# Kernel optimization log

Hardware: AMD Instinct MI355X
Metric: run time of the kernel (lower is better)

Reference implementation:

```python
import jax, jax.numpy as jnp
import numpy as np

D_MODEL = 4096
D_BASE = 8192
K_SUB = 1024
N_TOK = 8192


def setup_inputs() -> dict:
    key = jax.random.key(0)
    k1, k2, k3, k4 = jax.random.split(key, 4)
    x = jax.random.normal(k1, (N_TOK, D_MODEL), dtype=jnp.float32)
    subspace_indices = jax.random.randint(k2, (K_SUB,), 0, D_BASE)
    # learned shared basis (orthogonal init approximated by scaled gaussian)
    U_base = jax.random.normal(k3, (D_MODEL, D_BASE), dtype=jnp.float32) / np.sqrt(D_MODEL)
    V_base = jax.random.normal(k4, (D_BASE, D_MODEL), dtype=jnp.float32) / np.sqrt(D_BASE)
    return {"x": x, "subspace_indices": subspace_indices, "U_base": U_base, "V_base": V_base}


def reference(x, subspace_indices, U_base, V_base):
    # gather active subspace columns/rows of the shared basis
    u_subset = U_base[:, subspace_indices]          # [d_model, k]
    v_subset = V_base[subspace_indices, :]          # [k, d_model]
    projected = jax.nn.silu(x @ u_subset)           # [n_tok, k]
    return projected @ v_subset                     # [n_tok, d_model]
```

## Files before the change

### kernel.cpp

```cpp
#include <hip/hip_runtime.h>
#include <hip/hip_bf16.h>
#include <stdint.h>

#define D_MODEL 4096
#define D_BASE  8192
#define K_SUB   1024
#define N_TOK   8192

typedef __attribute__((ext_vector_type(8))) short bf16x8;
typedef __attribute__((ext_vector_type(4))) float f32x4;

__device__ __forceinline__ unsigned short f2bf(float f) {
    union { float f; uint32_t u; } c; c.f = f;
    uint32_t u = c.u;
    uint32_t r = u + 0x7FFFu + ((u >> 16) & 1u);
    return (unsigned short)(r >> 16);
}

__device__ __forceinline__ void gload_lds16(const void* g, void* l) {
    __builtin_amdgcn_global_load_lds(
        (__attribute__((address_space(1))) void*)g,
        (__attribute__((address_space(3))) void*)l, 16, 0, 0);
}

#define VMCNT(N) do { __builtin_amdgcn_sched_barrier(0); \
    asm volatile("s_waitcnt vmcnt(" #N ")" ::: "memory"); } while (0)
#define PHASE_MID() do { __builtin_amdgcn_sched_barrier(0); __builtin_amdgcn_s_barrier(); \
    asm volatile("s_waitcnt lgkmcnt(0)" ::: "memory"); __builtin_amdgcn_sched_barrier(0); } while (0)
#define PHASE_END() do { __builtin_amdgcn_sched_barrier(0); __builtin_amdgcn_s_barrier(); } while (0)

__global__ void convert_x_kernel(const float* __restrict__ x, unsigned short* __restrict__ xb) {
    int t = blockIdx.x * 256 + threadIdx.x;
    const float4* p = (const float4*)x + (size_t)t * 2;
    float4 a = p[0], b = p[1];
    ushort4 lo, hi;
    lo.x = f2bf(a.x); lo.y = f2bf(a.y); lo.z = f2bf(a.z); lo.w = f2bf(a.w);
    hi.x = f2bf(b.x); hi.y = f2bf(b.y); hi.z = f2bf(b.z); hi.w = f2bf(b.w);
    *(ushort4*)(xb + (size_t)t * 8) = lo;
    *(ushort4*)(xb + (size_t)t * 8 + 4) = hi;
}

__global__ __launch_bounds__(256) void gather_u_s(const float* __restrict__ U,
                                                  const int* __restrict__ idx,
                                                  unsigned short* __restrict__ Ut) {
    __shared__ unsigned short tile[1024 * 36];
    __shared__ int lidx[1024];
    const int t = threadIdx.x;
    const int k0 = blockIdx.x * 32;
    #pragma unroll
    for (int i = 0; i < 4; ++i) lidx[i * 256 + t] = idx[i * 256 + t];
    __syncthreads();
    for (int kr = 0; kr < 32; ++kr) {
        const float* Urow = U + (size_t)(k0 + kr) * D_BASE;
        #pragma unroll
        for (int it = 0; it < 4; ++it) {
            int n = it * 256 + t;
            tile[n * 36 + kr] = f2bf(Urow[lidx[n]]);
        }
    }
    __syncthreads();
    #pragma unroll
    for (int r = 0; r < 4; ++r) {
        int n = r * 256 + t;
        unsigned short* drow = Ut + (size_t)n * D_MODEL + k0;
        #pragma unroll
        for (int j = 0; j < 8; ++j) {
            ushort4 v = *(const ushort4*)&tile[n * 36 + j * 4];
            *(ushort4*)(drow + j * 4) = v;
        }
    }
}

__global__ __launch_bounds__(256) void gather_v_t(const float* __restrict__ V,
                                                  const int* __restrict__ idx,
                                                  unsigned short* __restrict__ Vt) {
    __shared__ unsigned short tile[64][66];
    __shared__ int lidx[64];
    const int t = threadIdx.x;
    const int n0 = (blockIdx.x & 15) * 64;
    const int d0 = (blockIdx.x >> 4) * 64;
    if (t < 64) lidx[t] = idx[n0 + t];
    __syncthreads();
    const int c = t & 63, r4 = t >> 6;
    #pragma unroll
    for (int p = 0; p < 16; ++p) {
        int nr = p * 4 + r4;
        tile[nr][c] = f2bf(V[(size_t)lidx[nr] * D_MODEL + d0 + c]);
    }
    __syncthreads();
    #pragma unroll
    for (int p = 0; p < 16; ++p) {
        int dr = p * 4 + r4;
        Vt[(size_t)(d0 + dr) * K_SUB + n0 + c] = tile[c][dr];
    }
}

__global__ __launch_bounds__(512, 2)
void gemm1_8p(const unsigned short* __restrict__ A, const unsigned short* __restrict__ Bt,
              unsigned short* __restrict__ C) {
    constexpr int K = D_MODEL, N = K_SUB, NT = K / 64;
    __shared__ __align__(16) unsigned short lds[49152];

    const int t = threadIdx.x, lane = t & 63, w = t >> 6;
    const int wm = w >> 1, wn = w & 1;
    const int lr = lane & 15, lk = lane >> 4;

    const int f = blockIdx.x;
    const int g = (f & 7) * 32 + (f >> 3);
    const int m0 = (g >> 3) * 256, n0 = (g & 7) * 128;

    const int cswz0 = ((lk ^ (lr & 7)) * 8);
    const int cswz1 = (((4 + lk) ^ (lr & 7)) * 8);
    const int srow = lane >> 3;
    const int scol = ((lane & 7) ^ srow) * 8;

    auto stage_A = [&](int kt, int half) {
        const unsigned short* src = A + (size_t)(m0 + half * 128) * K + kt * 64;
        unsigned short* dst = &lds[(kt & 1) * 24576 + half * 8192];
        #pragma unroll
        for (int i = 0; i < 2; ++i) {
            int c2 = i * 8 + w;
            gload_lds16(src + (size_t)(c2 * 8 + srow) * K + scol, dst + c2 * 512);
        }
    };
    auto stage_B = [&](int kt) {
        const unsigned short* src = Bt + (size_t)n0 * K + kt * 64;
        unsigned short* dst = &lds[(kt & 1) * 24576 + 16384];
        #pragma unroll
        for (int i = 0; i < 2; ++i) {
            int c2 = i * 8 + w;
            gload_lds16(src + (size_t)(c2 * 8 + srow) * K + scol, dst + c2 * 512);
        }
    };
    auto read_A = [&](int kt, bf16x8 (&af)[4][2]) {
        const unsigned short* base = &lds[(kt & 1) * 24576 + (wm >> 1) * 8192];
        #pragma unroll
        for (int m = 0; m < 4; ++m) {
            int rw = (wm & 1) * 64 + m * 16 + lr;
            af[m][0] = *(const bf16x8*)(base + rw * 64 + cswz0);
            af[m][1] = *(const bf16x8*)(base + rw * 64 + cswz1);
        }
    };
    auto read_B2 = [&](int kt, int nh, bf16x8 (&bfr)[2][2]) {
        const unsigned short* base = &lds[(kt & 1) * 24576 + 16384];
        #pragma unroll
        for (int n = 0; n < 2; ++n) {
            int rw = wn * 64 + (nh * 2 + n) * 16 + lr;
            bfr[n][0] = *(const bf16x8*)(base + rw * 64 + cswz0);
            bfr[n][1] = *(const bf16x8*)(base + rw * 64 + cswz1);
        }
    };

    f32x4 acc[4][4] = {};

    stage_A(0, 0); stage_A(0, 1); stage_B(0); stage_A(1, 0);
    VMCNT(2);
    __builtin_amdgcn_s_barrier();
    __builtin_amdgcn_sched_barrier(0);

    for (int kt = 0; kt < NT; kt += 2) {
        const bool more = (kt + 2 < NT);
        {
            bf16x8 af[4][2], bfr[2][2];
            read_A(kt, af); read_B2(kt, 0, bfr);
            stage_A(kt + 1, 1); stage_B(kt + 1);
            PHASE_MID();
            __builtin_amdgcn_s_setprio(1);
            #pragma unroll
            for (int m = 0; m < 4; ++m)
                #pragma unroll
                for (int n = 0; n < 2; ++n)
                    #pragma unroll
                    for (int ks = 0; ks < 2; ++ks)
                        acc[m][n] = __builtin_amdgcn_mfma_f32_16x16x32_bf16(
                            af[m][ks], bfr[n][ks], acc[m][n], 0, 0, 0);
            __builtin_amdgcn_s_setprio(0);
            PHASE_END();
            bf16x8 bfr2[2][2];
            read_B2(kt, 1, bfr2);
            if (more) stage_A(kt + 2, 0);
            PHASE_MID();
            __builtin_amdgcn_s_setprio(1);
            #pragma unroll
            for (int m = 0; m < 4; ++m)
                #pragma unroll
                for (int n = 0; n < 2; ++n)
                    #pragma unroll
                    for (int ks = 0; ks < 2; ++ks)
                        acc[m][2 + n] = __builtin_amdgcn_mfma_f32_16x16x32_bf16(
                            af[m][ks], bfr2[n][ks], acc[m][2 + n], 0, 0, 0);
            __builtin_amdgcn_s_setprio(0);
            if (more) { VMCNT(2); } else { VMCNT(0); }
            PHASE_END();
        }
        {
            bf16x8 af[4][2], bfr[2][2];
            read_A(kt + 1, af); read_B2(kt + 1, 0, bfr);
            if (more) { stage_A(kt + 2, 1); stage_B(kt + 2); }
            PHASE_MID();
            __builtin_amdgcn_s_setprio(1);
            #pragma unroll
            for (int m = 0; m < 4; ++m)
                #pragma unroll
                for (int n = 0; n < 2; ++n)
                    #pragma unroll
                    for (int ks = 0; ks < 2; ++ks)
                        acc[m][n] = __builtin_amdgcn_mfma_f32_16x16x32_bf16(
                            af[m][ks], bfr[n][ks], acc[m][n], 0, 0, 0);
            __builtin_amdgcn_s_setprio(0);
            PHASE_END();
            bf16x8 bfr2[2][2];
            read_B2(kt + 1, 1, bfr2);
            if (more) stage_A(kt + 3, 0);
            PHASE_MID();
            __builtin_amdgcn_s_setprio(1);
            #pragma unroll
            for (int m = 0; m < 4; ++m)
                #pragma unroll
                for (int n = 0; n < 2; ++n)
                    #pragma unroll
                    for (int ks = 0; ks < 2; ++ks)
                        acc[m][2 + n] = __builtin_amdgcn_mfma_f32_16x16x32_bf16(
                            af[m][ks], bfr2[n][ks], acc[m][2 + n], 0, 0, 0);
            __builtin_amdgcn_s_setprio(0);
            if (more) VMCNT(2);
            PHASE_END();
        }
    }

    #pragma unroll
    for (int m = 0; m < 4; ++m)
        #pragma unroll
        for (int n = 0; n < 4; ++n)
            #pragma unroll
            for (int r = 0; r < 4; ++r) {
                int row = m0 + wm * 64 + m * 16 + lk * 4 + r;
                int col = n0 + wn * 64 + n * 16 + lr;
                float v = acc[m][n][r];
                v = v / (1.0f + __expf(-v));
                C[(size_t)row * N + col] = f2bf(v);
            }
}

__global__ __launch_bounds__(512, 2)
void gemm2_8p(const unsigned short* __restrict__ A, const unsigned short* __restrict__ Bt,
              float* __restrict__ C) {
    constexpr int K = K_SUB, N = D_MODEL, NT = K / 64;
    constexpr int BUFSZ = 32768;
    __shared__ __align__(16) unsigned short lds[2 * BUFSZ];

    const int t = threadIdx.x, lane = t & 63, w = t >> 6;
    const int wr = w >> 2, wc = w & 3;
    const int lr = lane & 15, lk = lane >> 4;

    const int f = blockIdx.x;
    const int g = (f & 7) * 64 + (f >> 3);
    const int m0 = (g >> 4) * 256, n0 = (g & 15) * 256;

    const int cswz0 = ((lk ^ (lr & 7)) * 8);
    const int cswz1 = (((4 + lk) ^ (lr & 7)) * 8);
    const int srow = lane >> 3;
    const int scol = ((lane & 7) ^ srow) * 8;

    auto stage_A = [&](int kt, int mh) {
        const unsigned short* src = A + (size_t)(m0 + mh * 128) * K + kt * 64;
        unsigned short* dst = &lds[(kt & 1) * BUFSZ + mh * 8192];
        #pragma unroll
        for (int i = 0; i < 2; ++i) {
            int c2 = i * 8 + w;
            gload_lds16(src + (size_t)(c2 * 8 + srow) * K + scol, dst + c2 * 512);
        }
    };
    auto stage_B = [&](int kt, int nh) {
        const unsigned short* src = Bt + (size_t)(n0 + nh * 128) * K + kt * 64;
        unsigned short* dst = &lds[(kt & 1) * BUFSZ + 16384 + nh * 8192];
        #pragma unroll
        for (int i = 0; i < 2; ++i) {
            int c2 = i * 8 + w;
            gload_lds16(src + (size_t)(c2 * 8 + srow) * K + scol, dst + c2 * 512);
        }
    };
    auto read_A = [&](int kt, int mh, bf16x8 (&af)[4][2]) {
        const unsigned short* base = &lds[(kt & 1) * BUFSZ + mh * 8192];
        #pragma unroll
        for (int m = 0; m < 4; ++m) {
            int rw = wr * 64 + m * 16 + lr;
            af[m][0] = *(const bf16x8*)(base + rw * 64 + cswz0);
            af[m][1] = *(const bf16x8*)(base + rw * 64 + cswz1);
        }
    };
    auto read_B = [&](int kt, int nh, bf16x8 (&bfr)[2][2]) {
        const unsigned short* base = &lds[(kt & 1) * BUFSZ + 16384 + nh * 8192];
        #pragma unroll
        for (int n = 0; n < 2; ++n) {
            int rw = wc * 32 + n * 16 + lr;
            bfr[n][0] = *(const bf16x8*)(base + rw * 64 + cswz0);
            bfr[n][1] = *(const bf16x8*)(base + rw * 64 + cswz1);
        }
    };

    f32x4 acc[8][4] = {};

    stage_A(0, 0); stage_B(0, 0); stage_B(0, 1); stage_A(0, 1);
    stage_A(1, 0); stage_B(1, 1); stage_A(1, 1);
    VMCNT(6);
    __builtin_amdgcn_s_barrier();
    __builtin_amdgcn_sched_barrier(0);

    for (int kt = 0; kt < NT; ++kt) {
        bf16x8 af[4][2], bf0[2][2], bf1[2][2];
        {
            read_A(kt, 0, af); read_B(kt, 0, bf0);
            if (kt + 1 < NT) stage_B(kt + 1, 0);
            PHASE_MID();
            __builtin_amdgcn_s_setprio(1);
            #pragma unroll
            for (int m = 0; m < 4; ++m)
                #pragma unroll
                for (int n = 0; n < 2; ++n)
                    #pragma unroll
                    for (int ks = 0; ks < 2; ++ks)
                        acc[m][n] = __builtin_amdgcn_mfma_f32_16x16x32_bf16(
                            af[m][ks], bf0[n][ks], acc[m][n], 0, 0, 0);
            __builtin_amdgcn_s_setprio(0);
            PHASE_END();
        }
        {
            read_B(kt, 1, bf1);
            if (kt + 2 < NT) stage_A(kt + 2, 0);
            PHASE_MID();
            __builtin_amdgcn_s_setprio(1);
            #pragma unroll
            for (int m = 0; m < 4; ++m)
                #pragma unroll
                for (int n = 0; n < 2; ++n)
                    #pragma unroll
                    for (int ks = 0; ks < 2; ++ks)
                        acc[m][2 + n] = __builtin_amdgcn_mfma_f32_16x16x32_bf16(
                            af[m][ks], bf1[n][ks], acc[m][2 + n], 0, 0, 0);
            __builtin_amdgcn_s_setprio(0);
            PHASE_END();
        }
        {
            read_A(kt, 1, af);
            if (kt + 2 < NT) stage_B(kt + 2, 1);
            PHASE_MID();
            __builtin_amdgcn_s_setprio(1);
            #pragma unroll
            for (int m = 0; m < 4; ++m)
                #pragma unroll
                for (int n = 0; n < 2; ++n)
                    #pragma unroll
                    for (int ks = 0; ks < 2; ++ks)
                        acc[4 + m][n] = __builtin_amdgcn_mfma_f32_16x16x32_bf16(
                            af[m][ks], bf0[n][ks], acc[4 + m][n], 0, 0, 0);
            __builtin_amdgcn_s_setprio(0);
            PHASE_END();
        }
        {
            if (kt + 2 < NT) stage_A(kt + 2, 1);
            PHASE_MID();
            __builtin_amdgcn_s_setprio(1);
            #pragma unroll
            for (int m = 0; m < 4; ++m)
                #pragma unroll
                for (int n = 0; n < 2; ++n)
                    #pragma unroll
                    for (int ks = 0; ks < 2; ++ks)
                        acc[4 + m][2 + n] = __builtin_amdgcn_mfma_f32_16x16x32_bf16(
                            af[m][ks], bf1[n][ks], acc[4 + m][2 + n], 0, 0, 0);
            __builtin_amdgcn_s_setprio(0);
            __builtin_amdgcn_sched_barrier(0);
            if (kt < NT - 2) { VMCNT(6); }
            else if (kt == NT - 2) { VMCNT(0); }
            PHASE_END();
        }
    }

    #pragma unroll
    for (int mh = 0; mh < 2; ++mh)
        #pragma unroll
        for (int nh = 0; nh < 2; ++nh)
            #pragma unroll
            for (int m = 0; m < 4; ++m)
                #pragma unroll
                for (int n = 0; n < 2; ++n)
                    #pragma unroll
                    for (int r = 0; r < 4; ++r) {
                        int row = m0 + mh * 128 + wr * 64 + m * 16 + lk * 4 + r;
                        int col = n0 + nh * 128 + wc * 32 + n * 16 + lr;
                        C[(size_t)row * N + col] = acc[mh * 4 + m][nh * 2 + n][r];
                    }
}

extern "C" void kernel_launch(void* const* d_in, const int* in_sizes, int n_in,
                              void* d_out, int out_size, void* d_ws, size_t ws_size,
                              hipStream_t stream) {
    const float* x   = (const float*)d_in[0];
    const int*   idx = (const int*)d_in[1];
    const float* U   = (const float*)d_in[2];
    const float* V   = (const float*)d_in[3];
    float* out = (float*)d_out;

    unsigned short* Ut = (unsigned short*)d_ws;
    unsigned short* Vt = Ut + (size_t)K_SUB * D_MODEL;
    unsigned short* P  = Vt + (size_t)K_SUB * D_MODEL;
    unsigned short* xb = (unsigned short*)d_out;

    convert_x_kernel<<<(N_TOK * D_MODEL) / (256 * 8), 256, 0, stream>>>(x, xb);
    gather_u_s<<<D_MODEL / 32, 256, 0, stream>>>(U, idx, Ut);
    gather_v_t<<<(K_SUB / 64) * (D_MODEL / 64), 256, 0, stream>>>(V, idx, Vt);

    gemm1_8p<<<256, 512, 0, stream>>>(xb, Ut, P);
    gemm2_8p<<<512, 512, 0, stream>>>(P, Vt, out);
}
```

Baseline: 241.8 us.

## Switch GEMMs to 32x32x16 MFMA and fuse prep kernels into one launch

Both GEMM kernels replace the 16x16x32 bf16 MFMA tiles with 32x32x16 tiles, changing the LDS fragment reads, accumulator layout and epilogue indexing to match. The three preprocessing kernels (x conversion, U gather, V gather-transpose) are merged into a single launch dispatched by block index. The U gather is also rewritten to drop its LDS staging and write 4-element vectors directly. The aim is fewer MFMA issues and operand reads per FLOP and less launch overhead. In exchange, the U gather now does strided uncoalesced reads, and the larger accumulators raise register pressure.

```diff
diff --git a/kernel.cpp b/kernel.cpp
--- a/kernel.cpp
+++ b/kernel.cpp
@@ -8,7 +8,7 @@
 #define N_TOK   8192
 
 typedef __attribute__((ext_vector_type(8))) short bf16x8;
-typedef __attribute__((ext_vector_type(4))) float f32x4;
+typedef __attribute__((ext_vector_type(16))) float f32x16;
 
 __device__ __forceinline__ unsigned short f2bf(float f) {
     union { float f; uint32_t u; } c; c.f = f;
@@ -29,69 +29,60 @@
     asm volatile("s_waitcnt lgkmcnt(0)" ::: "memory"); __builtin_amdgcn_sched_barrier(0); } while (0)
 #define PHASE_END() do { __builtin_amdgcn_sched_barrier(0); __builtin_amdgcn_s_barrier(); } while (0)
 
-__global__ void convert_x_kernel(const float* __restrict__ x, unsigned short* __restrict__ xb) {
-    int t = blockIdx.x * 256 + threadIdx.x;
-    const float4* p = (const float4*)x + (size_t)t * 2;
-    float4 a = p[0], b = p[1];
-    ushort4 lo, hi;
-    lo.x = f2bf(a.x); lo.y = f2bf(a.y); lo.z = f2bf(a.z); lo.w = f2bf(a.w);
-    hi.x = f2bf(b.x); hi.y = f2bf(b.y); hi.z = f2bf(b.z); hi.w = f2bf(b.w);
-    *(ushort4*)(xb + (size_t)t * 8) = lo;
-    *(ushort4*)(xb + (size_t)t * 8 + 4) = hi;
-}
-
-__global__ __launch_bounds__(256) void gather_u_s(const float* __restrict__ U,
+__global__ __launch_bounds__(256) void prep_fused(const float* __restrict__ x,
                                                   const int* __restrict__ idx,
-                                                  unsigned short* __restrict__ Ut) {
-    __shared__ unsigned short tile[1024 * 36];
-    __shared__ int lidx[1024];
-    const int t = threadIdx.x;
-    const int k0 = blockIdx.x * 32;
-    #pragma unroll
-    for (int i = 0; i < 4; ++i) lidx[i * 256 + t] = idx[i * 256 + t];
-    __syncthreads();
-    for (int kr = 0; kr < 32; ++kr) {
-        const float* Urow = U + (size_t)(k0 + kr) * D_BASE;
-        #pragma unroll
-        for (int it = 0; it < 4; ++it) {
-            int n = it * 256 + t;
-            tile[n * 36 + kr] = f2bf(Urow[lidx[n]]);
-        }
-    }
-    __syncthreads();
-    #pragma unroll
-    for (int r = 0; r < 4; ++r) {
-        int n = r * 256 + t;
-        unsigned short* drow = Ut + (size_t)n * D_MODEL + k0;
-        #pragma unroll
-        for (int j = 0; j < 8; ++j) {
-            ushort4 v = *(const ushort4*)&tile[n * 36 + j * 4];
-            *(ushort4*)(drow + j * 4) = v;
-        }
-    }
-}
-
-__global__ __launch_bounds__(256) void gather_v_t(const float* __restrict__ V,
-                                                  const int* __restrict__ idx,
+                                                  const float* __restrict__ U,
+                                                  const float* __restrict__ V,
+                                                  unsigned short* __restrict__ xb,
+                                                  unsigned short* __restrict__ Ut,
                                                   unsigned short* __restrict__ Vt) {
     __shared__ unsigned short tile[64][66];
     __shared__ int lidx[64];
+    const int b = blockIdx.x;
     const int t = threadIdx.x;
-    const int n0 = (blockIdx.x & 15) * 64;
-    const int d0 = (blockIdx.x >> 4) * 64;
-    if (t < 64) lidx[t] = idx[n0 + t];
-    __syncthreads();
-    const int c = t & 63, r4 = t >> 6;
-    #pragma unroll
-    for (int p = 0; p < 16; ++p) {
-        int nr = p * 4 + r4;
-        tile[nr][c] = f2bf(V[(size_t)lidx[nr] * D_MODEL + d0 + c]);
-    }
-    __syncthreads();
-    #pragma unroll
-    for (int p = 0; p < 16; ++p) {
-        int dr = p * 4 + r4;
-        Vt[(size_t)(d0 + dr) * K_SUB + n0 + c] = tile[c][dr];
+    if (b < 256) {
+        const int nq = t >> 2, kq = t & 3;
+        const int k0 = b * 16 + kq * 4;
+        #pragma unroll
+        for (int c = 0; c < 16; ++c) {
+            int n = nq + 64 * c;
+            int col = idx[n];
+            const float* Ucol = U + (size_t)k0 * D_BASE + col;
+            ushort4 o;
+            o.x = f2bf(Ucol[0]);
+            o.y = f2bf(Ucol[(size_t)D_BASE]);
+            o.z = f2bf(Ucol[(size_t)2 * D_BASE]);
+            o.w = f2bf(Ucol[(size_t)3 * D_BASE]);
+            *(ushort4*)(Ut + (size_t)n * D_MODEL + k0) = o;
+        }
+    } else if (b < 256 + 1024) {
+        const int bx = b - 256;
+        const int n0 = (bx & 15) * 64;
+        const int d0 = (bx >> 4) * 64;
+        if (t < 64) lidx[t] = idx[n0 + t];
+        __syncthreads();
+        const int c = t & 63, r4 = t >> 6;
+        #pragma unroll
+        for (int p = 0; p < 16; ++p) {
+            int nr = p * 4 + r4;
+            tile[nr][c] = f2bf(V[(size_t)lidx[nr] * D_MODEL + d0 + c]);
+        }
+        __syncthreads();
+        #pragma unroll
+        for (int p = 0; p < 16; ++p) {
+            int dr = p * 4 + r4;
+            Vt[(size_t)(d0 + dr) * K_SUB + n0 + c] = tile[c][dr];
+        }
+    } else {
+        const int cb = b - 1280;
+        int e = cb * 256 + t;
+        const float4* p = (const float4*)x + (size_t)e * 2;
+        float4 a = p[0], q = p[1];
+        ushort4 lo, hi;
+        lo.x = f2bf(a.x); lo.y = f2bf(a.y); lo.z = f2bf(a.z); lo.w = f2bf(a.w);
+        hi.x = f2bf(q.x); hi.y = f2bf(q.y); hi.z = f2bf(q.z); hi.w = f2bf(q.w);
+        *(ushort4*)(xb + (size_t)e * 8) = lo;
+        *(ushort4*)(xb + (size_t)e * 8 + 4) = hi;
     }
 }
 
@@ -103,14 +94,12 @@
 
     const int t = threadIdx.x, lane = t & 63, w = t >> 6;
     const int wm = w >> 1, wn = w & 1;
-    const int lr = lane & 15, lk = lane >> 4;
+    const int l31 = lane & 31, lh = lane >> 5;
 
     const int f = blockIdx.x;
     const int g = (f & 7) * 32 + (f >> 3);
     const int m0 = (g >> 3) * 256, n0 = (g & 7) * 128;
 
-    const int cswz0 = ((lk ^ (lr & 7)) * 8);
-    const int cswz1 = (((4 + lk) ^ (lr & 7)) * 8);
     const int srow = lane >> 3;
     const int scol = ((lane & 7) ^ srow) * 8;
 
@@ -132,26 +121,29 @@
             gload_lds16(src + (size_t)(c2 * 8 + srow) * K + scol, dst + c2 * 512);
         }
     };
-    auto read_A = [&](int kt, bf16x8 (&af)[4][2]) {
+    auto read_A = [&](int kt, bf16x8 (&af)[2][4]) {
         const unsigned short* base = &lds[(kt & 1) * 24576 + (wm >> 1) * 8192];
         #pragma unroll
-        for (int m = 0; m < 4; ++m) {
-            int rw = (wm & 1) * 64 + m * 16 + lr;
-            af[m][0] = *(const bf16x8*)(base + rw * 64 + cswz0);
-            af[m][1] = *(const bf16x8*)(base + rw * 64 + cswz1);
-        }
-    };
-    auto read_B2 = [&](int kt, int nh, bf16x8 (&bfr)[2][2]) {
+        for (int mf = 0; mf < 2; ++mf) {
+            int rw = (wm & 1) * 64 + mf * 32 + l31;
+            #pragma unroll
+            for (int ks = 0; ks < 4; ++ks) {
+                int gg = ks * 2 + lh;
+                af[mf][ks] = *(const bf16x8*)(base + rw * 64 + ((gg ^ (rw & 7)) * 8));
+            }
+        }
+    };
+    auto read_B1 = [&](int kt, int nf, bf16x8 (&bfr)[4]) {
         const unsigned short* base = &lds[(kt & 1) * 24576 + 16384];
-        #pragma unroll
-        for (int n = 0; n < 2; ++n) {
-            int rw = wn * 64 + (nh * 2 + n) * 16 + lr;
-            bfr[n][0] = *(const bf16x8*)(base + rw * 64 + cswz0);
-            bfr[n][1] = *(const bf16x8*)(base + rw * 64 + cswz1);
-        }
-    };
-
-    f32x4 acc[4][4] = {};
+        int rw = wn * 64 + nf * 32 + l31;
+        #pragma unroll
+        for (int ks = 0; ks < 4; ++ks) {
+            int gg = ks * 2 + lh;
+            bfr[ks] = *(const bf16x8*)(base + rw * 64 + ((gg ^ (rw & 7)) * 8));
+        }
+    };
+
+    f32x16 acc[2][2] = {};
 
     stage_A(0, 0); stage_A(0, 1); stage_B(0); stage_A(1, 0);
     VMCNT(2);
@@ -161,67 +153,59 @@
     for (int kt = 0; kt < NT; kt += 2) {
         const bool more = (kt + 2 < NT);
         {
-            bf16x8 af[4][2], bfr[2][2];
-            read_A(kt, af); read_B2(kt, 0, bfr);
+            bf16x8 af[2][4], bfr[4];
+            read_A(kt, af); read_B1(kt, 0, bfr);
             stage_A(kt + 1, 1); stage_B(kt + 1);
             PHASE_MID();
             __builtin_amdgcn_s_setprio(1);
             #pragma unroll
-            for (int m = 0; m < 4; ++m)
-                #pragma unroll
-                for (int n = 0; n < 2; ++n)
-                    #pragma unroll
-                    for (int ks = 0; ks < 2; ++ks)
-                        acc[m][n] = __builtin_amdgcn_mfma_f32_16x16x32_bf16(
-                            af[m][ks], bfr[n][ks], acc[m][n], 0, 0, 0);
-            __builtin_amdgcn_s_setprio(0);
-            PHASE_END();
-            bf16x8 bfr2[2][2];
-            read_B2(kt, 1, bfr2);
+            for (int mf = 0; mf < 2; ++mf)
+                #pragma unroll
+                for (int ks = 0; ks < 4; ++ks)
+                    acc[mf][0] = __builtin_amdgcn_mfma_f32_32x32x16_bf16(
+                        af[mf][ks], bfr[ks], acc[mf][0], 0, 0, 0);
+            __builtin_amdgcn_s_setprio(0);
+            PHASE_END();
+            bf16x8 bfr2[4];
+            read_B1(kt, 1, bfr2);
             if (more) stage_A(kt + 2, 0);
             PHASE_MID();
             __builtin_amdgcn_s_setprio(1);
             #pragma unroll
-            for (int m = 0; m < 4; ++m)
-                #pragma unroll
-                for (int n = 0; n < 2; ++n)
-                    #pragma unroll
-                    for (int ks = 0; ks < 2; ++ks)
-                        acc[m][2 + n] = __builtin_amdgcn_mfma_f32_16x16x32_bf16(
-                            af[m][ks], bfr2[n][ks], acc[m][2 + n], 0, 0, 0);
+            for (int mf = 0; mf < 2; ++mf)
+                #pragma unroll
+                for (int ks = 0; ks < 4; ++ks)
+                    acc[mf][1] = __builtin_amdgcn_mfma_f32_32x32x16_bf16(
+                        af[mf][ks], bfr2[ks], acc[mf][1], 0, 0, 0);
             __builtin_amdgcn_s_setprio(0);
             if (more) { VMCNT(2); } else { VMCNT(0); }
             PHASE_END();
         }
         {
-            bf16x8 af[4][2], bfr[2][2];
-            read_A(kt + 1, af); read_B2(kt + 1, 0, bfr);
+            bf16x8 af[2][4], bfr[4];
+            read_A(kt + 1, af); read_B1(kt + 1, 0, bfr);
             if (more) { stage_A(kt + 2, 1); stage_B(kt + 2); }
             PHASE_MID();
             __builtin_amdgcn_s_setprio(1);
             #pragma unroll
-            for (int m = 0; m < 4; ++m)
-                #pragma unroll
-                for (int n = 0; n < 2; ++n)
-                    #pragma unroll
-                    for (int ks = 0; ks < 2; ++ks)
-                        acc[m][n] = __builtin_amdgcn_mfma_f32_16x16x32_bf16(
-                            af[m][ks], bfr[n][ks], acc[m][n], 0, 0, 0);
-            __builtin_amdgcn_s_setprio(0);
-            PHASE_END();
-            bf16x8 bfr2[2][2];
-            read_B2(kt + 1, 1, bfr2);
+            for (int mf = 0; mf < 2; ++mf)
+                #pragma unroll
+                for (int ks = 0; ks < 4; ++ks)
+                    acc[mf][0] = __builtin_amdgcn_mfma_f32_32x32x16_bf16(
+                        af[mf][ks], bfr[ks], acc[mf][0], 0, 0, 0);
+            __builtin_amdgcn_s_setprio(0);
+            PHASE_END();
+            bf16x8 bfr2[4];
+            read_B1(kt + 1, 1, bfr2);
             if (more) stage_A(kt + 3, 0);
             PHASE_MID();
             __builtin_amdgcn_s_setprio(1);
             #pragma unroll
-            for (int m = 0; m < 4; ++m)
-                #pragma unroll
-                for (int n = 0; n < 2; ++n)
-                    #pragma unroll
-                    for (int ks = 0; ks < 2; ++ks)
-                        acc[m][2 + n] = __builtin_amdgcn_mfma_f32_16x16x32_bf16(
-                            af[m][ks], bfr2[n][ks], acc[m][2 + n], 0, 0, 0);
+            for (int mf = 0; mf < 2; ++mf)
+                #pragma unroll
+                for (int ks = 0; ks < 4; ++ks)
+                    acc[mf][1] = __builtin_amdgcn_mfma_f32_32x32x16_bf16(
+                        af[mf][ks], bfr2[ks], acc[mf][1], 0, 0, 0);
             __builtin_amdgcn_s_setprio(0);
             if (more) VMCNT(2);
             PHASE_END();
@@ -229,14 +213,14 @@
     }
 
     #pragma unroll
-    for (int m = 0; m < 4; ++m)
-        #pragma unroll
-        for (int n = 0; n < 4; ++n)
-            #pragma unroll
-            for (int r = 0; r < 4; ++r) {
-                int row = m0 + wm * 64 + m * 16 + lk * 4 + r;
-                int col = n0 + wn * 64 + n * 16 + lr;
-                float v = acc[m][n][r];
+    for (int mf = 0; mf < 2; ++mf)
+        #pragma unroll
+        for (int nf = 0; nf < 2; ++nf)
+            #pragma unroll
+            for (int j = 0; j < 16; ++j) {
+                int row = m0 + wm * 64 + mf * 32 + (j & 3) + 8 * (j >> 2) + 4 * lh;
+                int col = n0 + wn * 64 + nf * 32 + l31;
+                float v = acc[mf][nf][j];
                 v = v / (1.0f + __expf(-v));
                 C[(size_t)row * N + col] = f2bf(v);
             }
@@ -251,14 +235,12 @@
 
     const int t = threadIdx.x, lane = t & 63, w = t >> 6;
     const int wr = w >> 2, wc = w & 3;
-    const int lr = lane & 15, lk = lane >> 4;
+    const int l31 = lane & 31, lh = lane >> 5;
 
     const int f = blockIdx.x;
     const int g = (f & 7) * 64 + (f >> 3);
     const int m0 = (g >> 4) * 256, n0 = (g & 15) * 256;
 
-    const int cswz0 = ((lk ^ (lr & 7)) * 8);
-    const int cswz1 = (((4 + lk) ^ (lr & 7)) * 8);
     const int srow = lane >> 3;
     const int scol = ((lane & 7) ^ srow) * 8;
 
@@ -280,26 +262,29 @@
             gload_lds16(src + (size_t)(c2 * 8 + srow) * K + scol, dst + c2 * 512);
         }
     };
-    auto read_A = [&](int kt, int mh, bf16x8 (&af)[4][2]) {
+    auto read_A = [&](int kt, int mh, bf16x8 (&af)[2][4]) {
         const unsigned short* base = &lds[(kt & 1) * BUFSZ + mh * 8192];
         #pragma unroll
-        for (int m = 0; m < 4; ++m) {
-            int rw = wr * 64 + m * 16 + lr;
-            af[m][0] = *(const bf16x8*)(base + rw * 64 + cswz0);
-            af[m][1] = *(const bf16x8*)(base + rw * 64 + cswz1);
-        }
-    };
-    auto read_B = [&](int kt, int nh, bf16x8 (&bfr)[2][2]) {
+        for (int mf = 0; mf < 2; ++mf) {
+            int rw = wr * 64 + mf * 32 + l31;
+            #pragma unroll
+            for (int ks = 0; ks < 4; ++ks) {
+                int gg = ks * 2 + lh;
+                af[mf][ks] = *(const bf16x8*)(base + rw * 64 + ((gg ^ (rw & 7)) * 8));
+            }
+        }
+    };
+    auto read_B = [&](int kt, int nh, bf16x8 (&bfr)[4]) {
         const unsigned short* base = &lds[(kt & 1) * BUFSZ + 16384 + nh * 8192];
-        #pragma unroll
-        for (int n = 0; n < 2; ++n) {
-            int rw = wc * 32 + n * 16 + lr;
-            bfr[n][0] = *(const bf16x8*)(base + rw * 64 + cswz0);
-            bfr[n][1] = *(const bf16x8*)(base + rw * 64 + cswz1);
-        }
-    };
-
-    f32x4 acc[8][4] = {};
+        int rw = wc * 32 + l31;
+        #pragma unroll
+        for (int ks = 0; ks < 4; ++ks) {
+            int gg = ks * 2 + lh;
+            bfr[ks] = *(const bf16x8*)(base + rw * 64 + ((gg ^ (rw & 7)) * 8));
+        }
+    };
+
+    f32x16 acc00[2] = {}, acc01[2] = {}, acc10[2] = {}, acc11[2] = {};
 
     stage_A(0, 0); stage_B(0, 0); stage_B(0, 1); stage_A(0, 1);
     stage_A(1, 0); stage_B(1, 1); stage_A(1, 1);
@@ -308,20 +293,18 @@
     __builtin_amdgcn_sched_barrier(0);
 
     for (int kt = 0; kt < NT; ++kt) {
-        bf16x8 af[4][2], bf0[2][2], bf1[2][2];
+        bf16x8 af[2][4], bf0[4], bf1[4];
         {
             read_A(kt, 0, af); read_B(kt, 0, bf0);
             if (kt + 1 < NT) stage_B(kt + 1, 0);
             PHASE_MID();
             __builtin_amdgcn_s_setprio(1);
             #pragma unroll
-            for (int m = 0; m < 4; ++m)
-                #pragma unroll
-                for (int n = 0; n < 2; ++n)
-                    #pragma unroll
-                    for (int ks = 0; ks < 2; ++ks)
-                        acc[m][n] = __builtin_amdgcn_mfma_f32_16x16x32_bf16(
-                            af[m][ks], bf0[n][ks], acc[m][n], 0, 0, 0);
+            for (int mf = 0; mf < 2; ++mf)
+                #pragma unroll
+                for (int ks = 0; ks < 4; ++ks)
+                    acc00[mf] = __builtin_amdgcn_mfma_f32_32x32x16_bf16(
+                        af[mf][ks], bf0[ks], acc00[mf], 0, 0, 0);
             __builtin_amdgcn_s_setprio(0);
             PHASE_END();
         }
@@ -331,13 +314,11 @@
             PHASE_MID();
             __builtin_amdgcn_s_setprio(1);
             #pragma unroll
-            for (int m = 0; m < 4; ++m)
-                #pragma unroll
-                for (int n = 0; n < 2; ++n)
-                    #pragma unroll
-                    for (int ks = 0; ks < 2; ++ks)
-                        acc[m][2 + n] = __builtin_amdgcn_mfma_f32_16x16x32_bf16(
-                            af[m][ks], bf1[n][ks], acc[m][2 + n], 0, 0, 0);
+            for (int mf = 0; mf < 2; ++mf)
+                #pragma unroll
+                for (int ks = 0; ks < 4; ++ks)
+                    acc01[mf] = __builtin_amdgcn_mfma_f32_32x32x16_bf16(
+                        af[mf][ks], bf1[ks], acc01[mf], 0, 0, 0);
             __builtin_amdgcn_s_setprio(0);
             PHASE_END();
         }
@@ -347,13 +328,11 @@
             PHASE_MID();
             __builtin_amdgcn_s_setprio(1);
             #pragma unroll
-            for (int m = 0; m < 4; ++m)
-                #pragma unroll
-                for (int n = 0; n < 2; ++n)
-                    #pragma unroll
-                    for (int ks = 0; ks < 2; ++ks)
-                        acc[4 + m][n] = __builtin_amdgcn_mfma_f32_16x16x32_bf16(
-                            af[m][ks], bf0[n][ks], acc[4 + m][n], 0, 0, 0);
+            for (int mf = 0; mf < 2; ++mf)
+                #pragma unroll
+                for (int ks = 0; ks < 4; ++ks)
+                    acc10[mf] = __builtin_amdgcn_mfma_f32_32x32x16_bf16(
+                        af[mf][ks], bf0[ks], acc10[mf], 0, 0, 0);
             __builtin_amdgcn_s_setprio(0);
             PHASE_END();
         }
@@ -362,13 +341,11 @@
             PHASE_MID();
             __builtin_amdgcn_s_setprio(1);
             #pragma unroll
-            for (int m = 0; m < 4; ++m)
-                #pragma unroll
-                for (int n = 0; n < 2; ++n)
-                    #pragma unroll
-                    for (int ks = 0; ks < 2; ++ks)
-                        acc[4 + m][2 + n] = __builtin_amdgcn_mfma_f32_16x16x32_bf16(
-                            af[m][ks], bf1[n][ks], acc[4 + m][2 + n], 0, 0, 0);
+            for (int mf = 0; mf < 2; ++mf)
+                #pragma unroll
+                for (int ks = 0; ks < 4; ++ks)
+                    acc11[mf] = __builtin_amdgcn_mfma_f32_32x32x16_bf16(
+                        af[mf][ks], bf1[ks], acc11[mf], 0, 0, 0);
             __builtin_amdgcn_s_setprio(0);
             __builtin_amdgcn_sched_barrier(0);
             if (kt < NT - 2) { VMCNT(6); }
@@ -378,19 +355,16 @@
     }
 
     #pragma unroll
-    for (int mh = 0; mh < 2; ++mh)
-        #pragma unroll
-        for (int nh = 0; nh < 2; ++nh)
-            #pragma unroll
-            for (int m = 0; m < 4; ++m)
-                #pragma unroll
-                for (int n = 0; n < 2; ++n)
-                    #pragma unroll
-                    for (int r = 0; r < 4; ++r) {
-                        int row = m0 + mh * 128 + wr * 64 + m * 16 + lk * 4 + r;
-                        int col = n0 + nh * 128 + wc * 32 + n * 16 + lr;
-                        C[(size_t)row * N + col] = acc[mh * 4 + m][nh * 2 + n][r];
-                    }
+    for (int mf = 0; mf < 2; ++mf)
+        #pragma unroll
+        for (int j = 0; j < 16; ++j) {
+            int rbase = (j & 3) + 8 * (j >> 2) + 4 * lh + mf * 32 + wr * 64;
+            int cbase = wc * 32 + l31;
+            C[(size_t)(m0 + rbase) * N + (n0 + cbase)]             = acc00[mf][j];
+            C[(size_t)(m0 + rbase) * N + (n0 + 128 + cbase)]       = acc01[mf][j];
+            C[(size_t)(m0 + 128 + rbase) * N + (n0 + cbase)]       = acc10[mf][j];
+            C[(size_t)(m0 + 128 + rbase) * N + (n0 + 128 + cbase)] = acc11[mf][j];
+        }
 }
 
 extern "C" void kernel_launch(void* const* d_in, const int* in_sizes, int n_in,
@@ -407,10 +381,7 @@
     unsigned short* P  = Vt + (size_t)K_SUB * D_MODEL;
     unsigned short* xb = (unsigned short*)d_out;
 
-    convert_x_kernel<<<(N_TOK * D_MODEL) / (256 * 8), 256, 0, stream>>>(x, xb);
-    gather_u_s<<<D_MODEL / 32, 256, 0, stream>>>(U, idx, Ut);
-    gather_v_t<<<(K_SUB / 64) * (D_MODEL / 64), 256, 0, stream>>>(V, idx, Vt);
-
+    prep_fused<<<256 + 1024 + 16384, 256, 0, stream>>>(x, idx, U, V, xb, Ut, Vt);
     gemm1_8p<<<256, 512, 0, stream>>>(xb, Ut, P);
     gemm2_8p<<<512, 512, 0, stream>>>(P, Vt, out);
 }
```

Result: slower. 254.5 us (+5.2%).
